# Kernel optimization log

Measured on AMD Instinct MI355X. Metric: run time of the kernel, lower is better.

Reference implementation:

```python
import jax, jax.numpy as jnp
import numpy as np

EMBED_DIM = 1024
NUM_HEADS = 16
HEAD_DIM = EMBED_DIM // NUM_HEADS
FF_DIM = 4096
EPS = 1e-5


def layer_norm(x, gamma, beta):
    mu = jnp.mean(x, axis=-1, keepdims=True)
    var = jnp.var(x, axis=-1, keepdims=True)
    return (x - mu) * jax.lax.rsqrt(var + EPS) * gamma + beta


def setup_inputs() -> dict:
    key = jax.random.key(0)
    ks = jax.random.split(key, 10)
    B, S = 2, 2048
    sd = 1.0 / np.sqrt(EMBED_DIM)
    sf = 1.0 / np.sqrt(FF_DIM)
    return {
        "x": jax.random.normal(ks[0], (B, S, EMBED_DIM), jnp.float32),
        # grouped QKV: 3*num_heads groups, each embed_dim -> head_dim
        "Wqkv": jax.random.normal(ks[1], (3 * NUM_HEADS, EMBED_DIM, HEAD_DIM), jnp.float32) * sd,
        "bqkv": jnp.zeros((3 * NUM_HEADS, HEAD_DIM), jnp.float32),
        "Wo": jax.random.normal(ks[2], (EMBED_DIM, EMBED_DIM), jnp.float32) * sd,
        "bo": jnp.zeros((EMBED_DIM,), jnp.float32),
        "W1": jax.random.normal(ks[3], (EMBED_DIM, FF_DIM), jnp.float32) * sd,
        "b1": jnp.zeros((FF_DIM,), jnp.float32),
        "W2": jax.random.normal(ks[4], (FF_DIM, EMBED_DIM), jnp.float32) * sf,
        "b2": jnp.zeros((EMBED_DIM,), jnp.float32),
        "ln1_g": jnp.ones((EMBED_DIM,), jnp.float32),
        "ln1_b": jnp.zeros((EMBED_DIM,), jnp.float32),
        "ln2_g": jnp.ones((EMBED_DIM,), jnp.float32),
        "ln2_b": jnp.zeros((EMBED_DIM,), jnp.float32),
    }


def reference(x, Wqkv, bqkv, Wo, bo, W1, b1, W2, b2, ln1_g, ln1_b, ln2_g, ln2_b):
    B, S, D = x.shape
    normed = layer_norm(x, ln1_g, ln1_b)
    # grouped QKV projection: group g gets its own (D, head_dim) weight
    qkv = jnp.einsum('bsd,gdh->bgsh', normed, Wqkv) + bqkv[None, :, None, :]
    qkv = qkv.reshape(B, 3, NUM_HEADS, S, HEAD_DIM)
    q, k, v = qkv[:, 0], qkv[:, 1], qkv[:, 2]  # each [B, H, S, hd]
    attn = jnp.einsum('bhqd,bhkd->bhqk', q, k) / np.sqrt(HEAD_DIM)
    attn = jax.nn.softmax(attn, axis=-1)
    out = jnp.einsum('bhqk,bhkd->bhqd', attn, v)
    out = out.transpose(0, 2, 1, 3).reshape(B, S, D)
    out = out @ Wo + bo
    x = x + out
    normed2 = layer_norm(x, ln2_g, ln2_b)
    ff = jax.nn.relu(normed2 @ W1 + b1) @ W2 + b2
    return x + ff
```

## Files before the change

kernel.cpp:

```cpp
#include <hip/hip_runtime.h>
#include <stdint.h>

#define SEQ    2048
#define NB     2
#define NHEADS 16
#define HDIM   64
#define EMBED  1024
#define NROWS  (NB*SEQ)
#define QKVSZ  ((size_t)NB*NHEADS*SEQ*HDIM)

typedef __attribute__((ext_vector_type(8))) short short8;
typedef __attribute__((ext_vector_type(4))) float float4v;
typedef __attribute__((ext_vector_type(16))) float float16v;
typedef __attribute__((ext_vector_type(2))) unsigned int uint2v;
typedef __attribute__((ext_vector_type(4))) unsigned int uint4v;

__device__ __forceinline__ float b2f(unsigned short h) {
    unsigned int u = ((unsigned int)h) << 16;
    union { unsigned int u; float f; } c; c.u = u; return c.f;
}
__device__ __forceinline__ unsigned short f2b(float f) {
    union { float f; unsigned int u; } c; c.f = f;
    unsigned int u = c.u;
    u += 0x7FFFu + ((u >> 16) & 1u);
    return (unsigned short)(u >> 16);
}
__device__ __forceinline__ unsigned int fbits(float f) {
    union { float f; unsigned int u; } c; c.f = f; return c.u;
}
__device__ __forceinline__ unsigned int cvtpk_bf16(float lo, float hi) {
    unsigned int r;
    asm("v_cvt_pk_bf16_f32 %0, %1, %2" : "=v"(r) : "v"(lo), "v"(hi));
    return r;
}

__device__ __forceinline__ void gload_lds16(const void* g, void* l) {
    __builtin_amdgcn_global_load_lds(
        (const __attribute__((address_space(1))) unsigned int*)g,
        (__attribute__((address_space(3))) unsigned int*)l, 16, 0, 0);
}

__device__ __forceinline__ int probe_f32(const void* probe) {
    return ((const unsigned short*)probe)[0] == 0;
}
__device__ __forceinline__ float lde(const void* base, size_t off, int f32) {
    return f32 ? ((const float*)base)[off] : b2f(((const unsigned short*)base)[off]);
}
__device__ __forceinline__ void ste(void* base, size_t off, float v, int f32) {
    if (f32) ((float*)base)[off] = v;
    else     ((unsigned short*)base)[off] = f2b(v);
}

__global__ __launch_bounds__(256) void ln_kernel(
    const void* __restrict__ x,
    const void* __restrict__ g,
    const void* __restrict__ b,
    unsigned short* __restrict__ out,
    const void* __restrict__ probe)
{
    int f32 = probe_f32(probe);
    int row = blockIdx.x;
    int t = threadIdx.x;
    float v0, v1, v2, v3;
    if (f32) {
        float4 rv = ((const float4*)x)[(size_t)row * (EMBED / 4) + t];
        v0 = rv.x; v1 = rv.y; v2 = rv.z; v3 = rv.w;
    } else {
        ushort4 rv = ((const ushort4*)((const unsigned short*)x + (size_t)row * EMBED))[t];
        v0 = b2f(rv.x); v1 = b2f(rv.y); v2 = b2f(rv.z); v3 = b2f(rv.w);
    }
    float s  = v0 + v1 + v2 + v3;
    float sq = v0*v0 + v1*v1 + v2*v2 + v3*v3;
    #pragma unroll
    for (int off = 32; off > 0; off >>= 1) {
        s  += __shfl_xor(s,  off);
        sq += __shfl_xor(sq, off);
    }
    __shared__ float red[8];
    int lane = t & 63, wv = t >> 6;
    if (lane == 0) { red[wv] = s; red[wv + 4] = sq; }
    __syncthreads();
    s  = red[0] + red[1] + red[2] + red[3];
    sq = red[4] + red[5] + red[6] + red[7];
    float mu  = s * (1.0f / EMBED);
    float var = sq * (1.0f / EMBED) - mu * mu;
    float rs  = rsqrtf(var + 1e-5f);
    float g0 = lde(g, t*4+0, f32), g1 = lde(g, t*4+1, f32);
    float g2 = lde(g, t*4+2, f32), g3 = lde(g, t*4+3, f32);
    float b0 = lde(b, t*4+0, f32), b1 = lde(b, t*4+1, f32);
    float b2 = lde(b, t*4+2, f32), b3 = lde(b, t*4+3, f32);
    ushort4 ov;
    ov.x = f2b((v0 - mu) * rs * g0 + b0);
    ov.y = f2b((v1 - mu) * rs * g1 + b1);
    ov.z = f2b((v2 - mu) * rs * g2 + b2);
    ov.w = f2b((v3 - mu) * rs * g3 + b3);
    ((ushort4*)(out + (size_t)row * EMBED))[t] = ov;
}

template<int QKV>
__global__ __launch_bounds__(256) void transpose_kernel(
    const void* __restrict__ in,
    unsigned short* __restrict__ out, int K, int N,
    const void* __restrict__ probe)
{
    __shared__ unsigned short t[64 * 68];
    int f32 = probe_f32(probe);
    int tid = threadIdx.x;
    int n0 = blockIdx.x * 64, k0 = blockIdx.y * 64;
    #pragma unroll
    for (int i = 0; i < 4; i++) {
        int id = tid + i * 256;
        int kr = id >> 4, nc = (id & 15) * 4;
        size_t srcoff;
        if (QKV) srcoff = ((size_t)(n0 >> 6) << 16) + (size_t)(k0 + kr) * 64 + nc;
        else     srcoff = (size_t)(k0 + kr) * N + n0 + nc;
        ushort4 val;
        if (f32) {
            float4 rv = *(const float4*)((const float*)in + srcoff);
            val.x = f2b(rv.x); val.y = f2b(rv.y); val.z = f2b(rv.z); val.w = f2b(rv.w);
        } else {
            val = *(const ushort4*)((const unsigned short*)in + srcoff);
        }
        *(ushort4*)&t[kr * 68 + nc] = val;
    }
    __syncthreads();
    #pragma unroll
    for (int i = 0; i < 4; i++) {
        int id = tid + i * 256;
        int nr = id >> 4, kc = (id & 15) * 4;
        ushort4 o;
        o.x = t[(kc + 0) * 68 + nr];
        o.y = t[(kc + 1) * 68 + nr];
        o.z = t[(kc + 2) * 68 + nr];
        o.w = t[(kc + 3) * 68 + nr];
        *(ushort4*)(out + (size_t)(n0 + nr) * K + k0 + kc) = o;
    }
}

template<int DO_RELU, int HAS_BIAS, int OUTMODE>
__global__ __launch_bounds__(512) void gemm256_kernel(
    const unsigned short* __restrict__ A,
    const unsigned short* __restrict__ Bt,
    const void* __restrict__ bias,
    void* __restrict__ out,
    int M, int N, int Kloc, int ldA, int ldB,
    const void* __restrict__ probe)
{
    __shared__ unsigned short Als[2][256 * 64];
    __shared__ unsigned short Bls[2][256 * 64];
    int f32 = probe_f32(probe);
    int tid = threadIdx.x;
    int lane = tid & 63, wv = tid >> 6;
    int lq = lane >> 4, lr = lane & 15;
    int wr = wv >> 2, wc = wv & 3;
    int m0 = blockIdx.y * 256, n0 = blockIdx.x * 256;
    int k0 = blockIdx.z * Kloc;

    int srow = tid >> 3;
    int sch  = (tid & 7) ^ (srow & 7);
    const unsigned short* ga = A  + (size_t)(m0 + srow) * ldA + k0 + sch * 8;
    const unsigned short* gb = Bt + (size_t)(n0 + srow) * ldB + k0 + sch * 8;
    int ldst = tid * 8;
    int rx = lr & 7;

    float4v acc[8][4];
    #pragma unroll
    for (int i = 0; i < 8; i++)
        #pragma unroll
        for (int j = 0; j < 4; j++)
            { acc[i][j][0] = 0.f; acc[i][j][1] = 0.f; acc[i][j][2] = 0.f; acc[i][j][3] = 0.f; }

    int nkt = Kloc >> 6;
    #pragma unroll
    for (int u = 0; u < 4; u++)
        gload_lds16(ga + (size_t)u * 64 * ldA, &Als[0][u * 4096 + ldst]);
    #pragma unroll
    for (int u = 0; u < 4; u++)
        gload_lds16(gb + (size_t)u * 64 * ldB, &Bls[0][u * 4096 + ldst]);

    for (int kt = 0; kt < nkt; kt++) {
        int cur = kt & 1, nxt = cur ^ 1;
        if (kt + 1 < nkt) {
            int ko = (kt + 1) * 64;
            #pragma unroll
            for (int u = 0; u < 4; u++)
                gload_lds16(ga + (size_t)u * 64 * ldA + ko, &Als[nxt][u * 4096 + ldst]);
            asm volatile("s_waitcnt vmcnt(4)" ::: "memory");
        } else {
            asm volatile("s_waitcnt vmcnt(0)" ::: "memory");
        }
        __builtin_amdgcn_s_barrier();
        asm volatile("" ::: "memory");
        {
            short8 af[8], bf[4];
            #pragma unroll
            for (int mt = 0; mt < 8; mt++)
                af[mt] = *(const short8*)(
                    &Als[cur][(wr * 128 + mt * 16 + lr) * 64 + ((lq ^ rx) * 8)]);
            #pragma unroll
            for (int nt = 0; nt < 4; nt++)
                bf[nt] = *(const short8*)(
                    &Bls[cur][(wc * 64 + nt * 16 + lr) * 64 + ((lq ^ rx) * 8)]);
            __builtin_amdgcn_s_setprio(1);
            #pragma unroll
            for (int mt = 0; mt < 8; mt++)
                #pragma unroll
                for (int nt = 0; nt < 4; nt++)
                    acc[mt][nt] = __builtin_amdgcn_mfma_f32_16x16x32_bf16(af[mt], bf[nt], acc[mt][nt], 0, 0, 0);
            __builtin_amdgcn_s_setprio(0);
        }
        if (kt + 1 < nkt) {
            int ko = (kt + 1) * 64;
            #pragma unroll
            for (int u = 0; u < 4; u++)
                gload_lds16(gb + (size_t)u * 64 * ldB + ko, &Bls[nxt][u * 4096 + ldst]);
        }
        {
            short8 af[8], bf[4];
            #pragma unroll
            for (int mt = 0; mt < 8; mt++)
                af[mt] = *(const short8*)(
                    &Als[cur][(wr * 128 + mt * 16 + lr) * 64 + (((4 + lq) ^ rx) * 8)]);
            #pragma unroll
            for (int nt = 0; nt < 4; nt++)
                bf[nt] = *(const short8*)(
                    &Bls[cur][(wc * 64 + nt * 16 + lr) * 64 + (((4 + lq) ^ rx) * 8)]);
            __builtin_amdgcn_s_setprio(1);
            #pragma unroll
            for (int mt = 0; mt < 8; mt++)
                #pragma unroll
                for (int nt = 0; nt < 4; nt++)
                    acc[mt][nt] = __builtin_amdgcn_mfma_f32_16x16x32_bf16(af[mt], bf[nt], acc[mt][nt], 0, 0, 0);
            __builtin_amdgcn_s_setprio(0);
        }
        asm volatile("s_waitcnt lgkmcnt(0)" ::: "memory");
        __builtin_amdgcn_s_barrier();
    }

    if (OUTMODE == 3) {
        float* po = (float*)out + (size_t)blockIdx.z * M * N;
        #pragma unroll
        for (int mt = 0; mt < 8; mt++)
            #pragma unroll
            for (int nt = 0; nt < 4; nt++)
                #pragma unroll
                for (int rg = 0; rg < 4; rg++) {
                    int rr = m0 + wr * 128 + mt * 16 + lq * 4 + rg;
                    int cc = n0 + wc * 64 + nt * 16 + lr;
                    po[(size_t)rr * N + cc] = acc[mt][nt][rg];
                }
    } else if (OUTMODE == 2) {
        #pragma unroll
        for (int mt = 0; mt < 8; mt++) {
            int rrb = m0 + wr * 128 + mt * 16 + lq * 4;
            int bb = rrb >> 11, ss = rrb & 2047;
            #pragma unroll
            for (int nt = 0; nt < 4; nt++) {
                int cc = n0 + wc * 64 + nt * 16 + lr;
                int gg = cc >> 6, hd = cc & 63;
                int ty = gg >> 4, hh = gg & 15;
                float vv[4];
                #pragma unroll
                for (int rg = 0; rg < 4; rg++) {
                    float v = acc[mt][nt][rg];
                    if (HAS_BIAS) v += lde(bias, (size_t)cc, f32);
                    vv[rg] = v;
                }
                if (ty < 2) {
                    unsigned short* p = (unsigned short*)out + (size_t)ty * QKVSZ +
                        (((size_t)(bb * NHEADS + hh) * SEQ + ss) * HDIM) + hd;
                    #pragma unroll
                    for (int rg = 0; rg < 4; rg++) p[(size_t)rg * HDIM] = f2b(vv[rg]);
                } else {
                    ushort4 pk;
                    pk.x = f2b(vv[0]); pk.y = f2b(vv[1]);
                    pk.z = f2b(vv[2]); pk.w = f2b(vv[3]);
                    *(ushort4*)((unsigned short*)out + 2 * QKVSZ +
                        ((size_t)(bb * NHEADS + hh) * HDIM + hd) * SEQ + ss) = pk;
                }
            }
        }
    } else {
        #pragma unroll
        for (int mt = 0; mt < 8; mt++)
            #pragma unroll
            for (int nt = 0; nt < 4; nt++)
                #pragma unroll
                for (int rg = 0; rg < 4; rg++) {
                    int rr = m0 + wr * 128 + mt * 16 + lq * 4 + rg;
                    int cc = n0 + wc * 64 + nt * 16 + lr;
                    float v = acc[mt][nt][rg];
                    if (HAS_BIAS) v += lde(bias, (size_t)cc, f32);
                    if (DO_RELU) v = v > 0.f ? v : 0.f;
                    ((unsigned short*)out)[(size_t)rr * N + cc] = f2b(v);
                }
    }
}

template<int DO_RELU, int HAS_BIAS, int OUTMODE>
__global__ __launch_bounds__(512) void gemm256p8_kernel(
    const unsigned short* __restrict__ A,
    const unsigned short* __restrict__ Bt,
    const void* __restrict__ bias,
    void* __restrict__ out,
    int M, int N, int Kloc, int ldA, int ldB,
    const void* __restrict__ probe)
{
    __shared__ unsigned short Als[2][2][128 * 64];
    __shared__ unsigned short Bls[2][2][128 * 64];
    int f32 = probe_f32(probe);
    int tid = threadIdx.x;
    int lane = tid & 63, wv = tid >> 6;
    int lq = lane >> 4, lr = lane & 15;
    int wr = wv >> 2, wc = wv & 3;
    int m0 = blockIdx.y * 256, n0 = blockIdx.x * 256;
    int k0 = blockIdx.z * Kloc;

    int srow = tid >> 3;
    int sch  = (tid & 7) ^ (srow & 7);
    const unsigned short* ga = A  + (size_t)(m0 + srow) * ldA + k0 + sch * 8;
    const unsigned short* gb = Bt + (size_t)(n0 + srow) * ldB + k0 + sch * 8;
    int ldst = tid * 8;
    int rx = lr & 7;

    auto stA = [&](int d, int h, int ko) {
        gload_lds16(ga + (size_t)(h * 128) * ldA + ko, &Als[d][h][ldst]);
        gload_lds16(ga + (size_t)(h * 128 + 64) * ldA + ko, &Als[d][h][4096 + ldst]);
    };
    auto stB = [&](int d, int h, int ko) {
        gload_lds16(gb + (size_t)(h * 128) * ldB + ko, &Bls[d][h][ldst]);
        gload_lds16(gb + (size_t)(h * 128 + 64) * ldB + ko, &Bls[d][h][4096 + ldst]);
    };
    auto rdA = [&](int d, int qm, short8 (&af)[4][2]) {
        #pragma unroll
        for (int mt = 0; mt < 4; mt++)
            #pragma unroll
            for (int c = 0; c < 2; c++)
                af[mt][c] = *(const short8*)(&Als[d][qm][
                    (wr * 64 + mt * 16 + lr) * 64 + (((c * 4 + lq) ^ rx) * 8)]);
    };
    auto rdB = [&](int d, int qn, short8 (&bf)[2][2]) {
        #pragma unroll
        for (int nt = 0; nt < 2; nt++)
            #pragma unroll
            for (int c = 0; c < 2; c++)
                bf[nt][c] = *(const short8*)(&Bls[d][qn][
                    (wc * 32 + nt * 16 + lr) * 64 + (((c * 4 + lq) ^ rx) * 8)]);
    };
    auto MM = [&](short8 (&af)[4][2], short8 (&bf)[2][2], float4v (&aq)[4][2]) {
        __builtin_amdgcn_s_setprio(1);
        #pragma unroll
        for (int c = 0; c < 2; c++)
            #pragma unroll
            for (int mt = 0; mt < 4; mt++)
                #pragma unroll
                for (int nt = 0; nt < 2; nt++)
                    aq[mt][nt] = __builtin_amdgcn_mfma_f32_16x16x32_bf16(
                        af[mt][c], bf[nt][c], aq[mt][nt], 0, 0, 0);
        __builtin_amdgcn_s_setprio(0);
    };
    #define VMC(n)  asm volatile("s_waitcnt vmcnt(" #n ")" ::: "memory")
    #define BARF()  do { __builtin_amdgcn_s_barrier(); \
                         asm volatile("" ::: "memory"); } while (0)

    float4v acc00[4][2], acc01[4][2], acc11[4][2], acc10[4][2];
    #pragma unroll
    for (int i = 0; i < 4; i++)
        #pragma unroll
        for (int j = 0; j < 2; j++) {
            acc00[i][j] = float4v{0.f, 0.f, 0.f, 0.f};
            acc01[i][j] = float4v{0.f, 0.f, 0.f, 0.f};
            acc11[i][j] = float4v{0.f, 0.f, 0.f, 0.f};
            acc10[i][j] = float4v{0.f, 0.f, 0.f, 0.f};
        }
    short8 af0[4][2], af1[4][2], bf0[2][2], bf1[2][2];

    int nkt = Kloc >> 6;
    int npair = nkt >> 1;

    stA(0, 0, 0); stB(0, 0, 0); stB(0, 1, 0); stA(0, 1, 0);
    VMC(4); BARF();
    rdA(0, 0, af0); rdB(0, 0, bf0);

    for (int p = 0; p < npair - 1; p++) {
        int koB  = (2 * p + 1) * 64;
        int koA2 = (2 * p + 2) * 64;
        MM(af0, bf0, acc00); stA(1, 0, koB); VMC(4); BARF(); rdB(0, 1, bf1);
        MM(af0, bf1, acc01); stB(1, 0, koB); VMC(4); BARF(); rdA(0, 1, af1);
        MM(af1, bf1, acc11); stB(1, 1, koB);         BARF(); rdB(0, 0, bf0);
        MM(af1, bf0, acc10); stA(1, 1, koB); VMC(4); BARF(); rdA(1, 0, af0); rdB(1, 0, bf1);
        MM(af0, bf1, acc00); stA(0, 0, koA2); VMC(4); BARF(); rdB(1, 1, bf0);
        MM(af0, bf0, acc01); stB(0, 0, koA2); VMC(4); BARF(); rdA(1, 1, af1);
        MM(af1, bf0, acc11); stB(0, 1, koA2);         BARF(); rdB(1, 0, bf1);
        MM(af1, bf1, acc10); stA(0, 1, koA2); VMC(4); BARF(); rdA(0, 0, af0); rdB(0, 0, bf0);
    }
    {
        int koB = (nkt - 1) * 64;
        MM(af0, bf0, acc00); stA(1, 0, koB); VMC(4); BARF(); rdB(0, 1, bf1);
        MM(af0, bf1, acc01); stB(1, 0, koB); VMC(4); BARF(); rdA(0, 1, af1);
        MM(af1, bf1, acc11); stB(1, 1, koB);         BARF(); rdB(0, 0, bf0);
        MM(af1, bf0, acc10); stA(1, 1, koB); VMC(4); BARF(); rdA(1, 0, af0); rdB(1, 0, bf1);
        MM(af0, bf1, acc00);                  VMC(2); BARF(); rdB(1, 1, bf0);
        MM(af0, bf0, acc01);                  VMC(0); BARF(); rdA(1, 1, af1);
        MM(af1, bf0, acc11);                          BARF(); rdB(1, 0, bf1);
        MM(af1, bf1, acc10);
    }
    #undef VMC
    #undef BARF

    auto storeQ = [&](int qr, int qc, float4v (&aq)[4][2]) {
        if (OUTMODE == 3) {
            float* po = (float*)out + (size_t)blockIdx.z * M * N;
            #pragma unroll
            for (int mt = 0; mt < 4; mt++)
                #pragma unroll
                for (int nt = 0; nt < 2; nt++)
                    #pragma unroll
                    for (int rg = 0; rg < 4; rg++) {
                        int rr = m0 + qr * 128 + wr * 64 + mt * 16 + lq * 4 + rg;
                        int cc = n0 + qc * 128 + wc * 32 + nt * 16 + lr;
                        po[(size_t)rr * N + cc] = aq[mt][nt][rg];
                    }
        } else {
            #pragma unroll
            for (int mt = 0; mt < 4; mt++)
                #pragma unroll
                for (int nt = 0; nt < 2; nt++)
                    #pragma unroll
                    for (int rg = 0; rg < 4; rg++) {
                        int rr = m0 + qr * 128 + wr * 64 + mt * 16 + lq * 4 + rg;
                        int cc = n0 + qc * 128 + wc * 32 + nt * 16 + lr;
                        float v = aq[mt][nt][rg];
                        if (HAS_BIAS) v += lde(bias, (size_t)cc, f32);
                        if (DO_RELU) v = v > 0.f ? v : 0.f;
                        ((unsigned short*)out)[(size_t)rr * N + cc] = f2b(v);
                    }
        }
    };
    storeQ(0, 0, acc00); storeQ(0, 1, acc01);
    storeQ(1, 1, acc11); storeQ(1, 0, acc10);
}

__global__ __launch_bounds__(256) void ff2_combine_kernel(
    const float* __restrict__ part,
    const void* __restrict__ b2,
    void* __restrict__ xout,
    const void* __restrict__ probe)
{
    int f32 = probe_f32(probe);
    int row = blockIdx.x;
    int t = threadIdx.x;
    const size_t MN = (size_t)NROWS * EMBED;
    size_t base = (size_t)row * EMBED + t * 4;
    float4 p0 = *(const float4*)(part + base);
    float4 p1 = *(const float4*)(part + MN + base);
    float4 p2 = *(const float4*)(part + 2 * MN + base);
    float4 p3 = *(const float4*)(part + 3 * MN + base);
    float s0 = (p0.x + p1.x) + (p2.x + p3.x);
    float s1 = (p0.y + p1.y) + (p2.y + p3.y);
    float s2 = (p0.z + p1.z) + (p2.z + p3.z);
    float s3 = (p0.w + p1.w) + (p2.w + p3.w);
    int c = t * 4;
    s0 += lde(b2, c + 0, f32) + lde(xout, base + 0, f32);
    s1 += lde(b2, c + 1, f32) + lde(xout, base + 1, f32);
    s2 += lde(b2, c + 2, f32) + lde(xout, base + 2, f32);
    s3 += lde(b2, c + 3, f32) + lde(xout, base + 3, f32);
    ste(xout, base + 0, s0, f32);
    ste(xout, base + 1, s1, f32);
    ste(xout, base + 2, s2, f32);
    ste(xout, base + 3, s3, f32);
}

template<int DO_RELU, int HAS_BIAS, int HAS_RES, int OUTMODE>
__global__ __launch_bounds__(256) void gemm64_kernel(
    const unsigned short* __restrict__ A,
    const unsigned short* __restrict__ Bt,
    const void* __restrict__ bias,
    const void* __restrict__ res,
    void* __restrict__ out,
    int M, int N, int K, int ldA, int ldB,
    const void* __restrict__ probe)
{
    __shared__ unsigned short Als[2][64 * 32];
    __shared__ unsigned short Bls[2][64 * 32];
    int f32 = probe_f32(probe);
    int tid = threadIdx.x;
    int lane = tid & 63, wv = tid >> 6;
    int lq = lane >> 4, lr = lane & 15;
    int moff = (wv >> 1) * 32, noff = (wv & 1) * 32;
    int m0 = blockIdx.y * 64, n0 = blockIdx.x * 64;

    int rA = tid >> 2, jA = tid & 3;
    int jjA = jA ^ ((rA >> 1) & 3);
    const unsigned short* ga = A  + (size_t)(m0 + rA) * ldA + jjA * 8;
    const unsigned short* gb = Bt + (size_t)(n0 + rA) * ldB + jjA * 8;

    int fch = (lq ^ ((lr >> 1) & 3)) * 8;

    float4v acc[2][2];
    #pragma unroll
    for (int i = 0; i < 2; i++)
        #pragma unroll
        for (int j = 0; j < 2; j++)
            { acc[i][j][0] = 0.f; acc[i][j][1] = 0.f; acc[i][j][2] = 0.f; acc[i][j][3] = 0.f; }

    gload_lds16(ga, &Als[0][(size_t)tid * 8]);
    gload_lds16(gb, &Bls[0][(size_t)tid * 8]);

    int nkt = K >> 5;
    for (int kt = 0; kt < nkt; kt++) {
        int cur = kt & 1, nxt = cur ^ 1;
        __syncthreads();
        if (kt + 1 < nkt) {
            int ko = (kt + 1) * 32;
            gload_lds16(ga + ko, &Als[nxt][(size_t)tid * 8]);
            gload_lds16(gb + ko, &Bls[nxt][(size_t)tid * 8]);
        }
        short8 af[2], bfr[2];
        #pragma unroll
        for (int mt = 0; mt < 2; mt++)
            af[mt] = *(const short8*)(&Als[cur][(moff + mt * 16 + lr) * 32 + fch]);
        #pragma unroll
        for (int nt = 0; nt < 2; nt++)
            bfr[nt] = *(const short8*)(&Bls[cur][(noff + nt * 16 + lr) * 32 + fch]);
        #pragma unroll
        for (int mt = 0; mt < 2; mt++)
            #pragma unroll
            for (int nt = 0; nt < 2; nt++)
                acc[mt][nt] = __builtin_amdgcn_mfma_f32_16x16x32_bf16(af[mt], bfr[nt], acc[mt][nt], 0, 0, 0);
    }

    #pragma unroll
    for (int mt = 0; mt < 2; mt++) {
        #pragma unroll
        for (int nt = 0; nt < 2; nt++) {
            #pragma unroll
            for (int rg = 0; rg < 4; rg++) {
                int rr = m0 + moff + mt * 16 + lq * 4 + rg;
                int cc = n0 + noff + nt * 16 + lr;
                float v = acc[mt][nt][rg];
                if (HAS_BIAS) v += lde(bias, (size_t)cc, f32);
                if (DO_RELU) v = v > 0.f ? v : 0.f;
                if (HAS_RES) v += lde(res, (size_t)rr * N + cc, f32);
                if (OUTMODE == 1) ste(out, (size_t)rr * N + cc, v, f32);
                else ((unsigned short*)out)[(size_t)rr * N + cc] = f2b(v);
            }
        }
    }
}

__global__ __launch_bounds__(256) void attn_kernel(
    const unsigned short* __restrict__ qb,
    const unsigned short* __restrict__ kb,
    const unsigned short* __restrict__ vtb,
    unsigned short* __restrict__ outb)
{
    __shared__ unsigned short Kls[2][64 * 64];
    __shared__ unsigned short Vls[2][64 * 64];
    int tid = threadIdx.x;
    int lane = tid & 63, wv = tid >> 6;
    int l31 = lane & 31, hh = lane >> 5;
    int bh = blockIdx.y;
    int b = bh >> 4, head = bh & 15;
    const unsigned short* q  = qb  + (size_t)bh * SEQ * HDIM;
    const unsigned short* k  = kb  + (size_t)bh * SEQ * HDIM;
    const unsigned short* vt = vtb + (size_t)bh * HDIM * SEQ;
    int q0w = blockIdx.x * 128 + wv * 32;

    const float C2 = 0.18033688011112042f;

    short8 qf[4];
    #pragma unroll
    for (int c = 0; c < 4; c++) {
        short8 raw = *(const short8*)(q + (size_t)(q0w + l31) * HDIM + c * 16 + hh * 8);
        #pragma unroll
        for (int j = 0; j < 8; j++)
            qf[c][j] = (short)f2b(b2f((unsigned short)raw[j]) * C2);
    }

    int rS = tid >> 3;
    int jjS = (tid & 7) ^ (rS & 7);
    const unsigned short* gk0 = k + (size_t)rS * HDIM + jjS * 8;
    const unsigned short* gk1 = k + (size_t)(rS + 32) * HDIM + jjS * 8;
    const unsigned short* gv0 = vt + (size_t)rS * SEQ + jjS * 8;
    const unsigned short* gv1 = vt + (size_t)(rS + 32) * SEQ + jjS * 8;

    float l_part = 0.f;
    float16v o0, o1;
    #pragma unroll
    for (int i = 0; i < 16; i++) { o0[i] = 0.f; o1[i] = 0.f; }

    gload_lds16(gk0, &Kls[0][(size_t)tid * 8]);
    gload_lds16(gk1, &Kls[0][(size_t)(tid + 256) * 8]);
    gload_lds16(gv0, &Vls[0][(size_t)tid * 8]);
    gload_lds16(gv1, &Vls[0][(size_t)(tid + 256) * 8]);

    for (int kt = 0; kt < SEQ / 64; kt++) {
        int cur = kt & 1, nxt = cur ^ 1;
        __syncthreads();
        if (kt + 1 < SEQ / 64) {
            int k0n = (kt + 1) * 64;
            gload_lds16(gk0 + (size_t)k0n * HDIM, &Kls[nxt][(size_t)tid * 8]);
            gload_lds16(gk1 + (size_t)k0n * HDIM, &Kls[nxt][(size_t)(tid + 256) * 8]);
            gload_lds16(gv0 + k0n, &Vls[nxt][(size_t)tid * 8]);
            gload_lds16(gv1 + k0n, &Vls[nxt][(size_t)(tid + 256) * 8]);
        }

        #pragma unroll
        for (int kb2 = 0; kb2 < 2; kb2++) {
            float16v st;
            #pragma unroll
            for (int i = 0; i < 16; i++) st[i] = 0.f;
            int r = kb2 * 32 + l31;
            int rx = r & 7;
            #pragma unroll
            for (int c = 0; c < 4; c++) {
                short8 kf = *(const short8*)(
                    &Kls[cur][r * 64 + (((2 * c + hh) ^ rx) * 8)]);
                st = __builtin_amdgcn_mfma_f32_32x32x16_bf16(kf, qf[c], st, 0, 0, 0);
            }
            float p[16];
            #pragma unroll
            for (int rg = 0; rg < 16; rg++) {
                p[rg] = __builtin_amdgcn_exp2f(st[rg]);
                l_part += p[rg];
            }
            int rv0 = l31, rv1 = 32 + l31;
            int rxv = l31 & 7;
            #pragma unroll
            for (int s = 0; s < 2; s++) {
                unsigned int a1 = cvtpk_bf16(p[8*s+0], p[8*s+1]);
                unsigned int a2 = cvtpk_bf16(p[8*s+2], p[8*s+3]);
                unsigned int b1 = cvtpk_bf16(p[8*s+4], p[8*s+5]);
                unsigned int b2 = cvtpk_bf16(p[8*s+6], p[8*s+7]);
                uint2v r1 = __builtin_amdgcn_permlane32_swap(a1, b1, false, false);
                uint2v r2 = __builtin_amdgcn_permlane32_swap(a2, b2, false, false);
                union { uint4v u; short8 s8; } pun;
                pun.u.x = r1.x; pun.u.y = r2.x; pun.u.z = r1.y; pun.u.w = r2.y;
                short8 pf = pun.s8;
                int g = kb2 * 2 + s;
                short8 vf0 = *(const short8*)(
                    &Vls[cur][rv0 * 64 + (((2 * g + hh) ^ rxv) * 8)]);
                o0 = __builtin_amdgcn_mfma_f32_32x32x16_bf16(pf, vf0, o0, 0, 0, 0);
                short8 vf1 = *(const short8*)(
                    &Vls[cur][rv1 * 64 + (((2 * g + hh) ^ rxv) * 8)]);
                o1 = __builtin_amdgcn_mfma_f32_32x32x16_bf16(pf, vf1, o1, 0, 0, 0);
            }
        }
    }

    l_part += __shfl_xor(l_part, 32);
    float linv_me = 1.f / l_part;
    #pragma unroll
    for (int rg = 0; rg < 16; rg++) {
        int qrow = (rg & 3) + 8 * (rg >> 2) + 4 * hh;
        float linv = __shfl(linv_me, qrow);
        size_t rowbase = ((size_t)(b * SEQ + q0w + qrow)) * EMBED + head * HDIM;
        outb[rowbase + l31]      = f2b(o0[rg] * linv);
        outb[rowbase + 32 + l31] = f2b(o1[rg] * linv);
    }
}

extern "C" void kernel_launch(void* const* d_in, const int* in_sizes, int n_in,
                              void* d_out, int out_size, void* d_ws, size_t ws_size,
                              hipStream_t stream)
{
    (void)in_sizes; (void)n_in; (void)out_size;
    const void* x    = d_in[0];
    const void* Wqkv = d_in[1];
    const void* bqkv = d_in[2];
    const void* Wo   = d_in[3];
    const void* bo   = d_in[4];
    const void* W1   = d_in[5];
    const void* b1   = d_in[6];
    const void* W2   = d_in[7];
    const void* b2   = d_in[8];
    const void* g1   = d_in[9];
    const void* be1  = d_in[10];
    const void* g2   = d_in[11];
    const void* be2  = d_in[12];
    const void* probe = g1;

    char* ws = (char*)d_ws;
    const size_t MB = 1024 * 1024;
    unsigned short* tmp1  = (unsigned short*)(ws + 0 * MB);
    unsigned short* qkv   = (unsigned short*)(ws + 8 * MB);
    unsigned short* WoT   = (unsigned short*)(ws + 8 * MB);
    unsigned short* W1T   = (unsigned short*)(ws + 8 * MB);
    unsigned short* W2T   = (unsigned short*)(ws + 8 * MB);
    unsigned short* h1    = (unsigned short*)(ws + 16 * MB);
    float*          part  = (float*)(ws + 48 * MB);
    unsigned short* WqkvT = (unsigned short*)d_out;
    bool splitk_ok = ws_size >= (size_t)112 * MB;

    transpose_kernel<1><<<dim3(3072 / 64, 1024 / 64), 256, 0, stream>>>(Wqkv, WqkvT, 1024, 3072, probe);
    ln_kernel<<<dim3(NROWS), 256, 0, stream>>>(x, g1, be1, tmp1, probe);
    gemm256_kernel<0, 1, 2><<<dim3(3072 / 256, NROWS / 256), 512, 0, stream>>>(
        tmp1, WqkvT, bqkv, qkv, NROWS, 3072, 1024, 1024, 1024, probe);
    attn_kernel<<<dim3(SEQ / 128, NB * NHEADS), 256, 0, stream>>>(
        qkv, qkv + QKVSZ, qkv + 2 * QKVSZ, tmp1);
    transpose_kernel<0><<<dim3(1024 / 64, 1024 / 64), 256, 0, stream>>>(Wo, WoT, 1024, 1024, probe);
    gemm64_kernel<0, 1, 1, 1><<<dim3(1024 / 64, NROWS / 64), 256, 0, stream>>>(
        tmp1, WoT, bo, x, d_out, NROWS, 1024, 1024, 1024, 1024, probe);
    ln_kernel<<<dim3(NROWS), 256, 0, stream>>>(d_out, g2, be2, tmp1, probe);
    transpose_kernel<0><<<dim3(4096 / 64, 1024 / 64), 256, 0, stream>>>(W1, W1T, 1024, 4096, probe);
    gemm256p8_kernel<1, 1, 0><<<dim3(4096 / 256, NROWS / 256), 512, 0, stream>>>(
        tmp1, W1T, b1, h1, NROWS, 4096, 1024, 1024, 1024, probe);
    transpose_kernel<0><<<dim3(1024 / 64, 4096 / 64), 256, 0, stream>>>(W2, W2T, 4096, 1024, probe);
    if (splitk_ok) {
        gemm256_kernel<0, 0, 3><<<dim3(1024 / 256, NROWS / 256, 4), 512, 0, stream>>>(
            h1, W2T, nullptr, part, NROWS, 1024, 1024, 4096, 4096, probe);
        ff2_combine_kernel<<<dim3(NROWS), 256, 0, stream>>>(part, b2, d_out, probe);
    } else {
        gemm64_kernel<0, 1, 1, 1><<<dim3(1024 / 64, NROWS / 64), 256, 0, stream>>>(
            h1, W2T, b2, d_out, d_out, NROWS, 1024, 4096, 4096, 4096, probe);
    }
}
```

Measured before the change: 388.7 us.

## Triple-buffer attention K/V tiles with vmcnt waits and swap FF2 GEMM variant

```diff
diff --git a/kernel.cpp b/kernel.cpp
--- a/kernel.cpp
+++ b/kernel.cpp
@@ -555,8 +555,8 @@
     const unsigned short* __restrict__ vtb,
     unsigned short* __restrict__ outb)
 {
-    __shared__ unsigned short Kls[2][64 * 64];
-    __shared__ unsigned short Vls[2][64 * 64];
+    __shared__ unsigned short Kls[3][64 * 64];
+    __shared__ unsigned short Vls[3][64 * 64];
     int tid = threadIdx.x;
     int lane = tid & 63, wv = tid >> 6;
     int l31 = lane & 31, hh = lane >> 5;
@@ -590,43 +590,59 @@
     #pragma unroll
     for (int i = 0; i < 16; i++) { o0[i] = 0.f; o1[i] = 0.f; }
 
-    gload_lds16(gk0, &Kls[0][(size_t)tid * 8]);
-    gload_lds16(gk1, &Kls[0][(size_t)(tid + 256) * 8]);
-    gload_lds16(gv0, &Vls[0][(size_t)tid * 8]);
-    gload_lds16(gv1, &Vls[0][(size_t)(tid + 256) * 8]);
-
-    for (int kt = 0; kt < SEQ / 64; kt++) {
-        int cur = kt & 1, nxt = cur ^ 1;
-        __syncthreads();
-        if (kt + 1 < SEQ / 64) {
-            int k0n = (kt + 1) * 64;
-            gload_lds16(gk0 + (size_t)k0n * HDIM, &Kls[nxt][(size_t)tid * 8]);
-            gload_lds16(gk1 + (size_t)k0n * HDIM, &Kls[nxt][(size_t)(tid + 256) * 8]);
-            gload_lds16(gv0 + k0n, &Vls[nxt][(size_t)tid * 8]);
-            gload_lds16(gv1 + k0n, &Vls[nxt][(size_t)(tid + 256) * 8]);
-        }
-
+    auto stage = [&](int bf, int kt) {
+        int k0n = kt * 64;
+        gload_lds16(gk0 + (size_t)k0n * HDIM, &Kls[bf][(size_t)tid * 8]);
+        gload_lds16(gk1 + (size_t)k0n * HDIM, &Kls[bf][(size_t)(tid + 256) * 8]);
+        gload_lds16(gv0 + k0n, &Vls[bf][(size_t)tid * 8]);
+        gload_lds16(gv1 + k0n, &Vls[bf][(size_t)(tid + 256) * 8]);
+    };
+
+    const int NT = SEQ / 64;
+    stage(0, 0);
+    stage(1, 1);
+
+    int cur = 0;
+    for (int kt = 0; kt < NT; kt++) {
+        if (kt + 1 < NT) asm volatile("s_waitcnt vmcnt(4)" ::: "memory");
+        else             asm volatile("s_waitcnt vmcnt(0)" ::: "memory");
+        __builtin_amdgcn_s_barrier();
+        asm volatile("" ::: "memory");
+        if (kt + 2 < NT) {
+            int nb = cur + 2; if (nb >= 3) nb -= 3;
+            stage(nb, kt + 2);
+        }
+
+        float16v st0, st1;
+        #pragma unroll
+        for (int i = 0; i < 16; i++) { st0[i] = 0.f; st1[i] = 0.f; }
+        {
+            int r0 = l31, r1 = 32 + l31;
+            int rxk = l31 & 7;
+            __builtin_amdgcn_s_setprio(1);
+            #pragma unroll
+            for (int c = 0; c < 4; c++) {
+                short8 kf0 = *(const short8*)(
+                    &Kls[cur][r0 * 64 + (((2 * c + hh) ^ rxk) * 8)]);
+                st0 = __builtin_amdgcn_mfma_f32_32x32x16_bf16(kf0, qf[c], st0, 0, 0, 0);
+                short8 kf1 = *(const short8*)(
+                    &Kls[cur][r1 * 64 + (((2 * c + hh) ^ rxk) * 8)]);
+                st1 = __builtin_amdgcn_mfma_f32_32x32x16_bf16(kf1, qf[c], st1, 0, 0, 0);
+            }
+            __builtin_amdgcn_s_setprio(0);
+        }
+
+        int rv0 = l31, rv1 = 32 + l31;
+        int rxv = l31 & 7;
         #pragma unroll
         for (int kb2 = 0; kb2 < 2; kb2++) {
-            float16v st;
-            #pragma unroll
-            for (int i = 0; i < 16; i++) st[i] = 0.f;
-            int r = kb2 * 32 + l31;
-            int rx = r & 7;
-            #pragma unroll
-            for (int c = 0; c < 4; c++) {
-                short8 kf = *(const short8*)(
-                    &Kls[cur][r * 64 + (((2 * c + hh) ^ rx) * 8)]);
-                st = __builtin_amdgcn_mfma_f32_32x32x16_bf16(kf, qf[c], st, 0, 0, 0);
-            }
             float p[16];
             #pragma unroll
             for (int rg = 0; rg < 16; rg++) {
-                p[rg] = __builtin_amdgcn_exp2f(st[rg]);
+                float sv = kb2 ? st1[rg] : st0[rg];
+                p[rg] = __builtin_amdgcn_exp2f(sv);
                 l_part += p[rg];
             }
-            int rv0 = l31, rv1 = 32 + l31;
-            int rxv = l31 & 7;
             #pragma unroll
             for (int s = 0; s < 2; s++) {
                 unsigned int a1 = cvtpk_bf16(p[8*s+0], p[8*s+1]);
@@ -641,12 +657,15 @@
                 int g = kb2 * 2 + s;
                 short8 vf0 = *(const short8*)(
                     &Vls[cur][rv0 * 64 + (((2 * g + hh) ^ rxv) * 8)]);
-                o0 = __builtin_amdgcn_mfma_f32_32x32x16_bf16(pf, vf0, o0, 0, 0, 0);
                 short8 vf1 = *(const short8*)(
                     &Vls[cur][rv1 * 64 + (((2 * g + hh) ^ rxv) * 8)]);
+                __builtin_amdgcn_s_setprio(1);
+                o0 = __builtin_amdgcn_mfma_f32_32x32x16_bf16(pf, vf0, o0, 0, 0, 0);
                 o1 = __builtin_amdgcn_mfma_f32_32x32x16_bf16(pf, vf1, o1, 0, 0, 0);
+                __builtin_amdgcn_s_setprio(0);
             }
         }
+        cur = cur + 1; if (cur >= 3) cur -= 3;
     }
 
     l_part += __shfl_xor(l_part, 32);
@@ -708,7 +727,7 @@
         tmp1, W1T, b1, h1, NROWS, 4096, 1024, 1024, 1024, probe);
     transpose_kernel<0><<<dim3(1024 / 64, 4096 / 64), 256, 0, stream>>>(W2, W2T, 4096, 1024, probe);
     if (splitk_ok) {
-        gemm256_kernel<0, 0, 3><<<dim3(1024 / 256, NROWS / 256, 4), 512, 0, stream>>>(
+        gemm256p8_kernel<0, 0, 3><<<dim3(1024 / 256, NROWS / 256, 4), 512, 0, stream>>>(
             h1, W2T, nullptr, part, NROWS, 1024, 1024, 4096, 4096, probe);
         ff2_combine_kernel<<<dim3(NROWS), 256, 0, stream>>>(part, b2, d_out, probe);
     } else {
```

New measurement: 386.5 us. Within noise of the previous version (-0.6%).
